# Kernel tuning notes

Hardware: AMD Instinct MI355X
Metric: run time of the kernel (lower is better)

The kernel has to match this reference:

```python
import jax, jax.numpy as jnp
import numpy as np

FACTOR = 3.0        # second_match_factor
MAX_DIST = 20.0     # second_match_max_dist
MATCHED_2 = 2       # SPIKE_MATCHED_2
CLID_UNMATCHED = 0

N, S, K = 1_000_000, 64, 32


def setup_inputs() -> dict:
    key = jax.random.key(0)
    k1, k2 = jax.random.split(key)
    return {
        "spikes": jax.random.normal(k1, (N, S), dtype=jnp.float32),
        "sort_idx": jax.random.randint(k2, (N,), 0, K, dtype=jnp.int32),
        "match_idx": jnp.zeros((N,), dtype=jnp.int32),
        "distance": jnp.zeros((N,), dtype=jnp.float32),
        "num_clusters": K,
    }


def reference(spikes, sort_idx, match_idx, distance, num_clusters):
    # spikes: (N, S) float32; sort_idx/match_idx: (N,) int; distance: (N,) float32
    n, s = spikes.shape
    k = int(num_clusters)

    # --- get_means: per-cluster mean waveform and scalar std (sqrt of summed per-dim variance)
    ones = jnp.ones((n,), spikes.dtype)
    counts = jax.ops.segment_sum(ones, sort_idx, num_segments=k)            # (K,)
    sums = jax.ops.segment_sum(spikes, sort_idx, num_segments=k)            # (K, S)
    sumsq = jax.ops.segment_sum(spikes * spikes, sort_idx, num_segments=k)  # (K, S)
    safe = jnp.maximum(counts, 1.0)[:, None]
    means = sums / safe                                                     # (K, S) templates
    var = sumsq / safe - means * means                                      # biased var (np.var ddof=0)
    stds = jnp.sqrt(jnp.maximum(var.sum(axis=1), 0.0))                      # (K,)
    valid = (jnp.arange(k) != CLID_UNMATCHED) & (counts > 0)                # exclude unmatched/empty

    x2 = (spikes * spikes).sum(axis=1, keepdims=True)                       # (N, 1)
    t2 = (means * means).sum(axis=1)                                        # (K,)
    d2 = x2 - 2.0 * (spikes @ means.T) + t2[None, :]
    dist = jnp.sqrt(jnp.maximum(d2, 1e-12))                                 # (N, K)

    # --- threshold mask (> factor*std -> inf) fused with invalid-cluster mask, then argmin
    inf = jnp.asarray(jnp.inf, dist.dtype)
    masked = jnp.where((dist > FACTOR * stds[None, :]) | ~valid[None, :], inf, dist)
    minima = masked.min(axis=1)                                             # (N,)
    minimizers = masked.argmin(axis=1).astype(sort_idx.dtype)               # cluster ids == segment ids
    minimizers = jnp.where(minima >= MAX_DIST * s, CLID_UNMATCHED, minimizers)

    # --- write back only for previously-unmatched spikes (the torch loop covers exactly these)
    unmatched = sort_idx == CLID_UNMATCHED
    new_sort = jnp.where(unmatched, minimizers, sort_idx)
    new_match = jnp.where(unmatched, MATCHED_2, match_idx)
    new_dist = jnp.where(unmatched, minima, distance)
    return new_sort, new_match, new_dist
```

## Files before the change

### kernel.cpp

```cpp
#include <hip/hip_runtime.h>
#include <math.h>

#define SDIM 64
#define KCL  32
#define NPART (KCL*SDIM*2 + KCL)
#define FACTOR_D 3.0
#define MAXDIST_TH 1280.0
#define MATCHED2_F 2.0f

#define SB 1024
#define ST 512

#define ACHUNK 512

__global__ __launch_bounds__(ST) void stats_kernel(
    const float* __restrict__ spikes, const int* __restrict__ sortidx,
    float* __restrict__ pws, int n, int chunk)
{
  const int lane  = threadIdx.x & 63;
  const int w     = threadIdx.x >> 6;
  const int cbase = w * 4;

  float s0=0,s1=0,s2=0,s3=0;
  float q0=0,q1=0,q2=0,q3=0;
  float cn0=0,cn1=0,cn2=0,cn3=0;

  const long long start = (long long)blockIdx.x * chunk;
  long long end = start + chunk; if (end > n) end = n;

  if (start < end) {
    long long il = start + lane;
    int id_cur = (il < end) ? sortidx[il] : -1;

    for (long long wb = start; wb < end; wb += 64) {
      const long long nl = wb + 64 + lane;
      const int id_next = (nl < end) ? sortidx[nl] : -1;

      unsigned long long m0 = __ballot(id_cur == cbase + 0);
      unsigned long long m1 = __ballot(id_cur == cbase + 1);
      unsigned long long m2 = __ballot(id_cur == cbase + 2);
      unsigned long long m3 = __ballot(id_cur == cbase + 3);
      if (w == 0) m0 = 0;

      cn0 += (float)__popcll(m0);
      cn1 += (float)__popcll(m1);
      cn2 += (float)__popcll(m2);
      cn3 += (float)__popcll(m3);

      while (m0 | m1 | m2 | m3) {
        const bool e0 = m0 != 0, e1 = m1 != 0, e2 = m2 != 0, e3 = m3 != 0;
        const int b0 = e0 ? __ffsll(m0) - 1 : 0;
        const int b1 = e1 ? __ffsll(m1) - 1 : 0;
        const int b2 = e2 ? __ffsll(m2) - 1 : 0;
        const int b3 = e3 ? __ffsll(m3) - 1 : 0;
        m0 &= m0 - 1; m1 &= m1 - 1; m2 &= m2 - 1; m3 &= m3 - 1;
        const float x0 = spikes[(size_t)(wb + b0) * SDIM + lane];
        const float x1 = spikes[(size_t)(wb + b1) * SDIM + lane];
        const float x2 = spikes[(size_t)(wb + b2) * SDIM + lane];
        const float x3 = spikes[(size_t)(wb + b3) * SDIM + lane];
        const float y0 = e0 ? x0 : 0.0f, y1 = e1 ? x1 : 0.0f;
        const float y2 = e2 ? x2 : 0.0f, y3 = e3 ? x3 : 0.0f;
        s0 += y0; q0 = fmaf(y0, x0, q0);
        s1 += y1; q1 = fmaf(y1, x1, q1);
        s2 += y2; q2 = fmaf(y2, x2, q2);
        s3 += y3; q3 = fmaf(y3, x3, q3);
      }
      id_cur = id_next;
    }
  }

  float* pb = pws + (size_t)blockIdx.x * NPART;
  pb[(cbase + 0) * SDIM + lane] = s0;
  pb[(cbase + 1) * SDIM + lane] = s1;
  pb[(cbase + 2) * SDIM + lane] = s2;
  pb[(cbase + 3) * SDIM + lane] = s3;
  pb[KCL * SDIM + (cbase + 0) * SDIM + lane] = q0;
  pb[KCL * SDIM + (cbase + 1) * SDIM + lane] = q1;
  pb[KCL * SDIM + (cbase + 2) * SDIM + lane] = q2;
  pb[KCL * SDIM + (cbase + 3) * SDIM + lane] = q3;
  if (lane == 0) {
    pb[2 * KCL * SDIM + cbase + 0] = cn0;
    pb[2 * KCL * SDIM + cbase + 1] = cn1;
    pb[2 * KCL * SDIM + cbase + 2] = cn2;
    pb[2 * KCL * SDIM + cbase + 3] = cn3;
  }
}

__global__ __launch_bounds__(1024) void reduce_kernel(
    const float* __restrict__ pws, double* __restrict__ gstats, int nb)
{
  __shared__ double s_acc[16][64];
  const int lane = threadIdx.x & 63;
  const int w    = threadIdx.x >> 6;
  const int u    = blockIdx.x * 64 + lane;
  double acc = 0.0;
  if (u < NPART)
    for (int b = w; b < nb; b += 16)
      acc += (double)pws[(size_t)b * NPART + u];
  s_acc[w][lane] = acc;
  __syncthreads();
  if (w == 0 && u < NPART) {
    double t = 0.0;
#pragma unroll
    for (int j = 0; j < 16; ++j) t += s_acc[j][lane];
    gstats[u] = t;
  }
}

__global__ __launch_bounds__(256) void finalize_kernel(
    const double* __restrict__ gstats, float* __restrict__ means_cs,
    double* __restrict__ t2, double* __restrict__ thr, int* __restrict__ validk)
{
  __shared__ double s_var[KCL], s_t2[KCL];
  if (threadIdx.x < KCL) { s_var[threadIdx.x] = 0.0; s_t2[threadIdx.x] = 0.0; }
  __syncthreads();
  const double* gsum = gstats;
  const double* gsq  = gstats + KCL * SDIM;
  const double* gcnt = gstats + 2 * KCL * SDIM;
  for (int i = threadIdx.x; i < KCL * SDIM; i += blockDim.x) {
    const int c = i / SDIM;
    const double cnt  = gcnt[c];
    const double safe = fmax(cnt, 1.0);
    const double m    = gsum[i] / safe;
    const double var  = gsq[i] / safe - m * m;
    means_cs[i] = (float)m;
    unsafeAtomicAdd(&s_var[c], var);
    unsafeAtomicAdd(&s_t2[c], m * m);
  }
  __syncthreads();
  if (threadIdx.x < KCL) {
    const int c = threadIdx.x;
    thr[c]    = FACTOR_D * sqrt(fmax(s_var[c], 0.0));
    t2[c]     = s_t2[c];
    validk[c] = (c != 0 && gcnt[c] > 0.0) ? 1 : 0;
  }
}

__global__ __launch_bounds__(256) void assign2_kernel(
    const float* __restrict__ spikes, const int* __restrict__ sortidx,
    const int* __restrict__ matchidx, const float* __restrict__ distance,
    const float* __restrict__ means_cs, const double* __restrict__ t2g,
    const double* __restrict__ thrg, const int* __restrict__ validk,
    float* __restrict__ out, int n)
{
  __shared__ float  s_m[KCL][SDIM];
  __shared__ double s_t2[KCL], s_thr[KCL];
  __shared__ int    s_valid[KCL];
  __shared__ int    ids[ACHUNK];
  __shared__ int    scnt;

  for (int i = threadIdx.x; i < KCL * SDIM; i += blockDim.x)
    (&s_m[0][0])[i] = means_cs[i];
  if (threadIdx.x < KCL) {
    s_t2[threadIdx.x]    = t2g[threadIdx.x];
    s_thr[threadIdx.x]   = thrg[threadIdx.x];
    s_valid[threadIdx.x] = validk[threadIdx.x];
  }
  if (threadIdx.x == 0) scnt = 0;
  __syncthreads();

  const long long start = (long long)blockIdx.x * ACHUNK;
  long long end = start + ACHUNK; if (end > n) end = n;

  for (long long i = start + threadIdx.x; i < end; i += blockDim.x) {
    const int cv = sortidx[i];
    if (cv != 0) {
      out[i]           = (float)cv;
      out[n + i]       = (float)matchidx[i];
      out[2LL * n + i] = distance[i];
    } else {
      const int p = atomicAdd(&scnt, 1);
      ids[p] = (int)i;
    }
  }
  __syncthreads();
  const int cnt = scnt;

  for (int base = 0; base < cnt; base += blockDim.x) {
    const int j = base + threadIdx.x;
    if (j >= cnt) break;
    const int r = ids[j];

    float4 xv[16];
    const float4* rp = reinterpret_cast<const float4*>(
        spikes + (size_t)r * SDIM);
#pragma unroll
    for (int s4 = 0; s4 < 16; ++s4) xv[s4] = rp[s4];

    float x2 = 0.0f;
#pragma unroll
    for (int s4 = 0; s4 < 16; ++s4) {
      x2 = fmaf(xv[s4].x, xv[s4].x, x2);
      x2 = fmaf(xv[s4].y, xv[s4].y, x2);
      x2 = fmaf(xv[s4].z, xv[s4].z, x2);
      x2 = fmaf(xv[s4].w, xv[s4].w, x2);
    }

    double best = (double)INFINITY;
    int bidx = 0;
    for (int c = 0; c < KCL; ++c) {
      float dot = 0.0f;
#pragma unroll
      for (int s4 = 0; s4 < 16; ++s4) {
        const float4 m = *reinterpret_cast<const float4*>(&s_m[c][s4 * 4]);
        dot = fmaf(xv[s4].x, m.x, dot);
        dot = fmaf(xv[s4].y, m.y, dot);
        dot = fmaf(xv[s4].z, m.z, dot);
        dot = fmaf(xv[s4].w, m.w, dot);
      }
      if (s_valid[c]) {
        const double d2 = (double)x2 - 2.0 * (double)dot + s_t2[c];
        double dist = sqrt(fmax(d2, 1e-12));
        if (dist <= s_thr[c] && dist < best) { best = dist; bidx = c; }
      }
    }

    const int mz = (best >= MAXDIST_TH) ? 0 : bidx;
    out[r]           = (float)mz;
    out[n + r]       = MATCHED2_F;
    out[2LL * n + r] = (float)best;
  }
}

extern "C" void kernel_launch(void* const* d_in, const int* in_sizes, int n_in,
                              void* d_out, int out_size, void* d_ws, size_t ws_size,
                              hipStream_t stream) {
  const float* spikes   = (const float*)d_in[0];
  const int*   sortidx  = (const int*)d_in[1];
  const int*   matchidx = (const int*)d_in[2];
  const float* distance = (const float*)d_in[3];
  const int n = in_sizes[1];
  if (n <= 0) return;
  float* out = (float*)d_out;

  float*  pws      = (float*)d_ws;
  double* gstats   = (double*)((char*)d_ws +
                               (((size_t)SB * NPART * sizeof(float) + 15) & ~15ull));
  float*  means_cs = (float*)(gstats + NPART);
  double* t2       = (double*)(((size_t)(means_cs + KCL * SDIM) + 7) & ~7ull);
  double* thr      = t2 + KCL;
  int*    validk   = (int*)(thr + KCL);

  const int chunk   = (int)((((long long)n + SB - 1) / SB + 63) & ~63LL);
  const int ablocks = (n + ACHUNK - 1) / ACHUNK;

  stats_kernel<<<SB, ST, 0, stream>>>(spikes, sortidx, pws, n, chunk);
  reduce_kernel<<<(NPART + 63) / 64, 1024, 0, stream>>>(pws, gstats, SB);
  finalize_kernel<<<1, 256, 0, stream>>>(gstats, means_cs, t2, thr, validk);
  assign2_kernel<<<ablocks, 256, 0, stream>>>(spikes, sortidx, matchidx,
                                              distance, means_cs, t2, thr,
                                              validk, out, n);
}
```

Measured before the change: 129.1 us.

## Give each wave its own row range and all clusters in stats kernel

The stats kernel changes from eight waves that each own four clusters and all scan the same rows to four waves that each scan a disjoint row range and accumulate all 32 clusters in registers. Each spike row is then read by a single wave instead of being ballot-scanned by eight, which cuts redundant sortidx and ballot work. Per-wave partial sums are combined in shared memory before one block partial is written. The cost is 96 register accumulators per lane, which may reduce occupancy or spill, plus a 31-iteration ballot loop per 64-row batch.

Result: slower. 218.0 us (+68.9%).

```diff
diff --git a/kernel.cpp b/kernel.cpp
--- a/kernel.cpp
+++ b/kernel.cpp
@@ -8,82 +8,99 @@
 #define MAXDIST_TH 1280.0
 #define MATCHED2_F 2.0f
 
-#define SB 1024
-#define ST 512
+#define SBLK 1024
+#define SWAVES 4
 
 #define ACHUNK 512
 
-__global__ __launch_bounds__(ST) void stats_kernel(
+__global__ __launch_bounds__(SWAVES * 64) void stats_kernel(
     const float* __restrict__ spikes, const int* __restrict__ sortidx,
-    float* __restrict__ pws, int n, int chunk)
-{
-  const int lane  = threadIdx.x & 63;
-  const int w     = threadIdx.x >> 6;
-  const int cbase = w * 4;
-
-  float s0=0,s1=0,s2=0,s3=0;
-  float q0=0,q1=0,q2=0,q3=0;
-  float cn0=0,cn1=0,cn2=0,cn3=0;
-
-  const long long start = (long long)blockIdx.x * chunk;
-  long long end = start + chunk; if (end > n) end = n;
-
-  if (start < end) {
-    long long il = start + lane;
-    int id_cur = (il < end) ? sortidx[il] : -1;
-
-    for (long long wb = start; wb < end; wb += 64) {
-      const long long nl = wb + 64 + lane;
-      const int id_next = (nl < end) ? sortidx[nl] : -1;
-
-      unsigned long long m0 = __ballot(id_cur == cbase + 0);
-      unsigned long long m1 = __ballot(id_cur == cbase + 1);
-      unsigned long long m2 = __ballot(id_cur == cbase + 2);
-      unsigned long long m3 = __ballot(id_cur == cbase + 3);
-      if (w == 0) m0 = 0;
-
-      cn0 += (float)__popcll(m0);
-      cn1 += (float)__popcll(m1);
-      cn2 += (float)__popcll(m2);
-      cn3 += (float)__popcll(m3);
-
-      while (m0 | m1 | m2 | m3) {
-        const bool e0 = m0 != 0, e1 = m1 != 0, e2 = m2 != 0, e3 = m3 != 0;
-        const int b0 = e0 ? __ffsll(m0) - 1 : 0;
-        const int b1 = e1 ? __ffsll(m1) - 1 : 0;
-        const int b2 = e2 ? __ffsll(m2) - 1 : 0;
-        const int b3 = e3 ? __ffsll(m3) - 1 : 0;
-        m0 &= m0 - 1; m1 &= m1 - 1; m2 &= m2 - 1; m3 &= m3 - 1;
-        const float x0 = spikes[(size_t)(wb + b0) * SDIM + lane];
-        const float x1 = spikes[(size_t)(wb + b1) * SDIM + lane];
-        const float x2 = spikes[(size_t)(wb + b2) * SDIM + lane];
-        const float x3 = spikes[(size_t)(wb + b3) * SDIM + lane];
-        const float y0 = e0 ? x0 : 0.0f, y1 = e1 ? x1 : 0.0f;
-        const float y2 = e2 ? x2 : 0.0f, y3 = e3 ? x3 : 0.0f;
-        s0 += y0; q0 = fmaf(y0, x0, q0);
-        s1 += y1; q1 = fmaf(y1, x1, q1);
-        s2 += y2; q2 = fmaf(y2, x2, q2);
-        s3 += y3; q3 = fmaf(y3, x3, q3);
+    float* __restrict__ pws, int n, int wchunk)
+{
+  const int lane = threadIdx.x & 63;
+  const int w    = threadIdx.x >> 6;
+
+  float sum[KCL], sq[KCL];
+#pragma unroll
+  for (int c = 0; c < KCL; ++c) { sum[c] = 0.0f; sq[c] = 0.0f; }
+  unsigned cnt[KCL];
+#pragma unroll
+  for (int c = 0; c < KCL; ++c) cnt[c] = 0u;
+
+  const long long wstart = (long long)(blockIdx.x * SWAVES + w) * wchunk;
+  long long wend = wstart + wchunk; if (wend > n) wend = n;
+
+  if (wstart < wend) {
+    int id_cur = (wstart + lane < wend) ? sortidx[wstart + lane] : -1;
+
+    for (long long wb = wstart; wb < wend; wb += 64) {
+      const long long nx = wb + 64 + lane;
+      const int id_next = (nx < wend) ? sortidx[nx] : -1;
+
+      const float* wrow = spikes + (size_t)wb * SDIM + lane;
+#pragma unroll
+      for (int c = 1; c < KCL; ++c) {
+        unsigned long long m = __ballot(id_cur == c);
+        if (m) {
+          cnt[c] += (unsigned)__popcll(m);
+          do {
+            const unsigned long long m1 = m & (m - 1);
+            const int b0 = __ffsll(m) - 1;
+            const bool e1 = m1 != 0;
+            const int b1 = e1 ? __ffsll(m1) - 1 : b0;
+            const float x0 = wrow[(size_t)b0 * SDIM];
+            const float x1 = wrow[(size_t)b1 * SDIM];
+            const float y1 = e1 ? x1 : 0.0f;
+            sum[c] += x0; sq[c] = fmaf(x0, x0, sq[c]);
+            sum[c] += y1; sq[c] = fmaf(y1, x1, sq[c]);
+            m = m1 & (m1 - 1);
+          } while (m);
+        }
       }
       id_cur = id_next;
     }
   }
 
+  __shared__ float red[2][NPART];
+
+#define WRSECT(BUF)                                                          \
+  {                                                                          \
+    _Pragma("unroll")                                                        \
+    for (int c = 0; c < KCL; ++c) {                                          \
+      red[BUF][c * SDIM + lane] = sum[c];                                    \
+      red[BUF][KCL * SDIM + c * SDIM + lane] = sq[c];                        \
+    }                                                                        \
+    float cv = 0.0f;                                                         \
+    _Pragma("unroll")                                                        \
+    for (int c = 0; c < KCL; ++c) if (lane == c) cv = (float)cnt[c];         \
+    if (lane < KCL) red[BUF][2 * KCL * SDIM + lane] = cv;                    \
+  }
+
+#define ADDSECT(BUF)                                                         \
+  {                                                                          \
+    _Pragma("unroll")                                                        \
+    for (int c = 0; c < KCL; ++c) {                                          \
+      red[BUF][c * SDIM + lane] += sum[c];                                   \
+      red[BUF][KCL * SDIM + c * SDIM + lane] += sq[c];                       \
+    }                                                                        \
+    float cv = 0.0f;                                                         \
+    _Pragma("unroll")                                                        \
+    for (int c = 0; c < KCL; ++c) if (lane == c) cv = (float)cnt[c];         \
+    if (lane < KCL) red[BUF][2 * KCL * SDIM + lane] += cv;                   \
+  }
+
+  if (w == 2) WRSECT(0)
+  if (w == 3) WRSECT(1)
+  __syncthreads();
+  if (w == 0) ADDSECT(0)
+  if (w == 1) ADDSECT(1)
+  __syncthreads();
+#undef WRSECT
+#undef ADDSECT
+
   float* pb = pws + (size_t)blockIdx.x * NPART;
-  pb[(cbase + 0) * SDIM + lane] = s0;
-  pb[(cbase + 1) * SDIM + lane] = s1;
-  pb[(cbase + 2) * SDIM + lane] = s2;
-  pb[(cbase + 3) * SDIM + lane] = s3;
-  pb[KCL * SDIM + (cbase + 0) * SDIM + lane] = q0;
-  pb[KCL * SDIM + (cbase + 1) * SDIM + lane] = q1;
-  pb[KCL * SDIM + (cbase + 2) * SDIM + lane] = q2;
-  pb[KCL * SDIM + (cbase + 3) * SDIM + lane] = q3;
-  if (lane == 0) {
-    pb[2 * KCL * SDIM + cbase + 0] = cn0;
-    pb[2 * KCL * SDIM + cbase + 1] = cn1;
-    pb[2 * KCL * SDIM + cbase + 2] = cn2;
-    pb[2 * KCL * SDIM + cbase + 3] = cn3;
-  }
+  for (int i = threadIdx.x; i < NPART; i += SWAVES * 64)
+    pb[i] = red[0][i] + red[1][i];
 }
 
 __global__ __launch_bounds__(1024) void reduce_kernel(
@@ -235,17 +252,18 @@
 
   float*  pws      = (float*)d_ws;
   double* gstats   = (double*)((char*)d_ws +
-                               (((size_t)SB * NPART * sizeof(float) + 15) & ~15ull));
+                               (((size_t)SBLK * NPART * sizeof(float) + 15) & ~15ull));
   float*  means_cs = (float*)(gstats + NPART);
   double* t2       = (double*)(((size_t)(means_cs + KCL * SDIM) + 7) & ~7ull);
   double* thr      = t2 + KCL;
   int*    validk   = (int*)(thr + KCL);
 
-  const int chunk   = (int)((((long long)n + SB - 1) / SB + 63) & ~63LL);
+  const int nw      = SBLK * SWAVES;
+  const int wchunk  = (int)((((long long)n + nw - 1) / nw + 63) & ~63LL);
   const int ablocks = (n + ACHUNK - 1) / ACHUNK;
 
-  stats_kernel<<<SB, ST, 0, stream>>>(spikes, sortidx, pws, n, chunk);
-  reduce_kernel<<<(NPART + 63) / 64, 1024, 0, stream>>>(pws, gstats, SB);
+  stats_kernel<<<SBLK, SWAVES * 64, 0, stream>>>(spikes, sortidx, pws, n, wchunk);
+  reduce_kernel<<<(NPART + 63) / 64, 1024, 0, stream>>>(pws, gstats, SBLK);
   finalize_kernel<<<1, 256, 0, stream>>>(gstats, means_cs, t2, thr, validk);
   assign2_kernel<<<ablocks, 256, 0, stream>>>(spikes, sortidx, matchidx,
                                               distance, means_cs, t2, thr,
```
